# Kernel tuning notes

Hardware: AMD Instinct MI355X
Metric: run time of the kernel (lower is better)

## Reference

```python
import jax, jax.numpy as jnp
import numpy as np

D = 1024

def setup_inputs() -> dict:
    key = jax.random.key(0)
    k1, k2, k3, k4, k5 = jax.random.split(key, 5)
    B, S = 128, 512
    seq_output = jax.random.normal(k1, (B, S, D), dtype=jnp.float32)
    mask = jax.random.randint(k2, (B, S), 0, 2) == 1  # True = masked position
    # ensure last position is never fully-masked pathological: fine either way
    scale1 = 1.0 / np.sqrt(D)
    W1 = jax.random.normal(k3, (D, D), dtype=jnp.float32) * scale1
    b1 = jnp.zeros((D,), dtype=jnp.float32)
    w2 = jax.random.normal(k4, (D,), dtype=jnp.float32) * scale1
    return {"seq_output": seq_output, "mask": mask, "W1": W1, "b1": b1, "w2": w2}

def reference(seq_output, mask, W1, b1, w2):
    # u_last: last timestep embedding
    u_last = seq_output[:, -1, :]                           # [B, D]
    # additive attention MLP: Linear -> tanh -> Linear(D->1, no bias)
    h = jnp.tanh(jnp.einsum('bsd,de->bse', seq_output, W1) + b1)  # [B, S, D]
    scores = jnp.einsum('bsd,d->bs', h, w2)                 # [B, S]
    scores = jnp.where(mask, -1e9, scores)
    attn = jax.nn.softmax(scores, axis=-1)                  # [B, S]
    u_att = jnp.einsum('bs,bsd->bd', attn, seq_output)      # [B, D]
    return (u_last, u_att)
```

## Files before the change

### kernel.cpp

```cpp
#include <hip/hip_runtime.h>
#include <hip/hip_bf16.h>
#include <cstdint>
#include <cstddef>

#define BATCH 128
#define SEQ   512
#define DIM   1024
#define MROWS (BATCH * SEQ)
#define NT    32

typedef short short8 __attribute__((ext_vector_type(8)));
typedef __bf16 bf16x8 __attribute__((ext_vector_type(8)));
typedef float f32x4 __attribute__((ext_vector_type(4)));

template <typename VA> struct other_frag { using type = bf16x8; };
template <> struct other_frag<bf16x8> { using type = short8; };

template <typename VA>
__device__ __forceinline__ auto try_mfma(VA a, VA b, f32x4 c, int)
    -> decltype(__builtin_amdgcn_mfma_f32_16x16x32_bf16(a, b, c, 0, 0, 0)) {
  return __builtin_amdgcn_mfma_f32_16x16x32_bf16(a, b, c, 0, 0, 0);
}
template <typename VA>
__device__ __forceinline__ f32x4 try_mfma(VA a, VA b, f32x4 c, long) {
  using O = typename other_frag<VA>::type;
  O a2 = __builtin_bit_cast(O, a);
  O b2 = __builtin_bit_cast(O, b);
  return __builtin_amdgcn_mfma_f32_16x16x32_bf16(a2, b2, c, 0, 0, 0);
}
__device__ __forceinline__ f32x4 mfma_bf16(short8 a, short8 b, f32x4 c) {
  return try_mfma(a, b, c, 0);
}

__device__ __forceinline__ unsigned short f32_to_bf16(float f) {
  union { float f; uint32_t u; } v; v.f = f;
  uint32_t u = v.u;
  u += 0x7FFFu + ((u >> 16) & 1u);
  return (unsigned short)(u >> 16);
}

__device__ __forceinline__ float bf16_to_f32(unsigned short u) {
  union { uint32_t u; float f; } v; v.u = ((uint32_t)u) << 16; return v.f;
}

__device__ __forceinline__ void gload_lds16(const void* g, void* l) {
  __builtin_amdgcn_global_load_lds(
      (__attribute__((address_space(1))) void*)g,
      (__attribute__((address_space(3))) void*)l,
      16, 0, 0);
}

__device__ __forceinline__ float fast_tanh(float x) {
  x = fminf(fmaxf(x, -15.0f), 15.0f);
  float e = __expf(2.0f * x);
  return (e - 1.0f) / (e + 1.0f);
}

__global__ __launch_bounds__(256) void cast_x_kernel(const float* __restrict__ X,
                                                     unsigned short* __restrict__ Xb) {
  const int total8 = MROWS * DIM / 8;
  int idx = blockIdx.x * 256 + threadIdx.x;
  const int stride = 2048 * 256;
  for (int i = idx; i < total8; i += stride) {
    const f32x4* p = (const f32x4*)X + (size_t)i * 2;
    f32x4 a = p[0];
    f32x4 b = p[1];
    short8 o;
    o[0] = (short)f32_to_bf16(a[0]); o[1] = (short)f32_to_bf16(a[1]);
    o[2] = (short)f32_to_bf16(a[2]); o[3] = (short)f32_to_bf16(a[3]);
    o[4] = (short)f32_to_bf16(b[0]); o[5] = (short)f32_to_bf16(b[1]);
    o[6] = (short)f32_to_bf16(b[2]); o[7] = (short)f32_to_bf16(b[3]);
    *((short8*)Xb + i) = o;
  }
}

__global__ __launch_bounds__(256) void w1t_kernel(const float* __restrict__ W1,
                                                  unsigned short* __restrict__ W1t) {
  __shared__ float tile[64][65];
  int bx = blockIdx.x & 15;
  int by = blockIdx.x >> 4;
  int t = threadIdx.x;
  int c = t & 63, r0 = t >> 6;
#pragma unroll
  for (int i = 0; i < 16; i++) {
    int r = i * 4 + r0;
    tile[r][c] = W1[(size_t)(by * 64 + r) * DIM + bx * 64 + c];
  }
  __syncthreads();
#pragma unroll
  for (int i = 0; i < 16; i++) {
    int r = i * 4 + r0;
    W1t[(size_t)(bx * 64 + r) * DIM + by * 64 + c] = f32_to_bf16(tile[c][r]);
  }
}

__global__ __launch_bounds__(256) void ulast_kernel(const float* __restrict__ X,
                                                    float* __restrict__ u_last) {
  int i = blockIdx.x * 256 + threadIdx.x;
  int b = i >> 8;
  int d4 = i & 255;
  ((f32x4*)u_last)[i] = ((const f32x4*)X)[((size_t)b * SEQ + (SEQ - 1)) * 256 + d4];
}

__global__ __launch_bounds__(512, 2) void gemm_score_kernel(
    const unsigned short* __restrict__ Xb,
    const unsigned short* __restrict__ W1t,
    const float* __restrict__ b1,
    const float* __restrict__ w2,
    float* __restrict__ scores) {
  __shared__ __align__(16) char lds[131072];

  const int tid = threadIdx.x;
  const int lane = tid & 63;
  const int w = tid >> 6;
  const int wr = w >> 2, wc = w & 3;

  const int bx = blockIdx.x;
  const int swz = (bx & 7) * 128 + (bx >> 3);
  const int m0 = (swz >> 2) * 256;
  const int n0 = (swz & 3) * 256;

  const unsigned short *a0Src, *a1Src, *b0Src, *b1Src;
  {
    int sc0 = w * 64 + lane;
    int sr0 = sc0 >> 3, j0 = (sc0 & 7) ^ (sr0 & 7);
    int row0 = sr0 * 2 + (j0 >> 2), c40 = j0 & 3;
    a0Src = Xb  + (size_t)(m0 + row0) * DIM + c40 * 8;
    b0Src = W1t + (size_t)(n0 + row0) * DIM + c40 * 8;
    int sc1 = (8 + w) * 64 + lane;
    int sr1 = sc1 >> 3, j1 = (sc1 & 7) ^ (sr1 & 7);
    int row1 = sr1 * 2 + (j1 >> 2), c41 = j1 & 3;
    a1Src = Xb  + (size_t)(m0 + row1) * DIM + c41 * 8;
    b1Src = W1t + (size_t)(n0 + row1) * DIM + c41 * 8;
  }
  const int dst0 = w * 1024;
  const int dst1 = (8 + w) * 1024;

  int aOff[8];
#pragma unroll
  for (int mi = 0; mi < 8; mi++) {
    int row = wr * 128 + mi * 16 + (lane & 15);
    int srow = row >> 1;
    int ic = ((row & 1) * 4 + (lane >> 4)) ^ (srow & 7);
    aOff[mi] = srow * 128 + ic * 16;
  }
  int bOff[4];
#pragma unroll
  for (int ni = 0; ni < 4; ni++) {
    int row = wc * 64 + ni * 16 + (lane & 15);
    int srow = row >> 1;
    int ic = ((row & 1) * 4 + (lane >> 4)) ^ (srow & 7);
    bOff[ni] = 65536 + srow * 128 + ic * 16;
  }

  f32x4 acc[8][4];
#pragma unroll
  for (int mi = 0; mi < 8; mi++)
#pragma unroll
    for (int ni = 0; ni < 4; ni++)
      acc[mi][ni] = (f32x4){0.f, 0.f, 0.f, 0.f};

#define STAGE(S) do {                                                   \
    const int bufS_ = ((S) & 3) * 16384;                                \
    const int ktS_ = (S) * 32;                                          \
    gload_lds16(a0Src + ktS_, lds + bufS_ + dst0);                      \
    gload_lds16(a1Src + ktS_, lds + bufS_ + dst1);                      \
    gload_lds16(b0Src + ktS_, lds + 65536 + bufS_ + dst0);              \
    gload_lds16(b1Src + ktS_, lds + 65536 + bufS_ + dst1);              \
  } while (0)

#define KITER(S, VMSTR) do {                                            \
    asm volatile("s_waitcnt vmcnt(" VMSTR ")" ::: "memory");            \
    __builtin_amdgcn_s_barrier();                                       \
    __builtin_amdgcn_sched_barrier(0);                                  \
    if ((S) + 3 < NT) STAGE((S) + 3);                                   \
    const int buf_ = ((S) & 3) * 16384;                                 \
    short8 af[8], bfv[4];                                               \
    _Pragma("unroll")                                                   \
    for (int mi = 0; mi < 8; mi++)                                      \
      af[mi] = *(const short8*)(lds + buf_ + aOff[mi]);                 \
    _Pragma("unroll")                                                   \
    for (int ni = 0; ni < 4; ni++)                                      \
      bfv[ni] = *(const short8*)(lds + buf_ + bOff[ni]);                \
    __builtin_amdgcn_s_setprio(1);                                      \
    _Pragma("unroll")                                                   \
    for (int mi = 0; mi < 8; mi++)                                      \
      _Pragma("unroll")                                                 \
      for (int ni = 0; ni < 4; ni++)                                    \
        acc[mi][ni] = mfma_bf16(af[mi], bfv[ni], acc[mi][ni]);          \
    __builtin_amdgcn_s_setprio(0);                                      \
  } while (0)

  STAGE(0); STAGE(1); STAGE(2);

  for (int s = 0; s < NT - 2; ++s) KITER(s, "8");
  KITER(NT - 2, "4");
  KITER(NT - 1, "0");

#undef STAGE
#undef KITER

  const int cg = lane >> 4;
  const int cl = lane & 15;
#pragma unroll
  for (int mi = 0; mi < 8; mi++) {
    float p0 = 0.f, p1 = 0.f, p2 = 0.f, p3 = 0.f;
#pragma unroll
    for (int ni = 0; ni < 4; ni++) {
      int col = n0 + wc * 64 + ni * 16 + cl;
      float w2v = w2[col];
      float b1v = b1[col];
      p0 += fast_tanh(acc[mi][ni][0] + b1v) * w2v;
      p1 += fast_tanh(acc[mi][ni][1] + b1v) * w2v;
      p2 += fast_tanh(acc[mi][ni][2] + b1v) * w2v;
      p3 += fast_tanh(acc[mi][ni][3] + b1v) * w2v;
    }
#pragma unroll
    for (int off = 1; off < 16; off <<= 1) {
      p0 += __shfl_xor(p0, off);
      p1 += __shfl_xor(p1, off);
      p2 += __shfl_xor(p2, off);
      p3 += __shfl_xor(p3, off);
    }
    if (cl == 0) {
      int row = m0 + wr * 128 + mi * 16 + cg * 4;
      atomicAdd(&scores[row + 0], p0);
      atomicAdd(&scores[row + 1], p1);
      atomicAdd(&scores[row + 2], p2);
      atomicAdd(&scores[row + 3], p3);
    }
  }
}

__global__ __launch_bounds__(256) void attn_uatt_kernel(
    const unsigned short* __restrict__ Xb,
    const float* __restrict__ scores,
    const int* __restrict__ mask,
    float* __restrict__ u_att) {
  const int b = blockIdx.x;
  const int half = blockIdx.y;
  const int tid = threadIdx.x;
  const int lane = tid & 63;
  const int wave = tid >> 6;

  __shared__ float attn[SEQ];
  __shared__ float rbuf[4];
  __shared__ float part[3][64 * 9];

  float s0 = scores[(size_t)b * SEQ + tid];
  float s1 = scores[(size_t)b * SEQ + 256 + tid];
  if (mask[(size_t)b * SEQ + tid]) s0 = -1000000000.0f;
  if (mask[(size_t)b * SEQ + 256 + tid]) s1 = -1000000000.0f;

  float mx = fmaxf(s0, s1);
#pragma unroll
  for (int off = 1; off < 64; off <<= 1) mx = fmaxf(mx, __shfl_xor(mx, off));
  if (lane == 0) rbuf[wave] = mx;
  __syncthreads();
  mx = fmaxf(fmaxf(rbuf[0], rbuf[1]), fmaxf(rbuf[2], rbuf[3]));

  float p0 = expf(s0 - mx), p1 = expf(s1 - mx);
  float sm = p0 + p1;
#pragma unroll
  for (int off = 1; off < 64; off <<= 1) sm += __shfl_xor(sm, off);
  __syncthreads();
  if (lane == 0) rbuf[wave] = sm;
  __syncthreads();
  sm = rbuf[0] + rbuf[1] + rbuf[2] + rbuf[3];
  float inv = 1.0f / sm;
  attn[tid] = p0 * inv;
  attn[tid + 256] = p1 * inv;
  __syncthreads();

  const int col = tid & 63;
  const int sh = tid >> 6;
  const short8* Xp = (const short8*)Xb + (size_t)b * SEQ * (DIM / 8) + half * 64 + col;
  float a[8] = {0.f, 0.f, 0.f, 0.f, 0.f, 0.f, 0.f, 0.f};
  for (int s = sh * 128; s < sh * 128 + 128; s++) {
    short8 v = Xp[(size_t)s * (DIM / 8)];
    float wgt = attn[s];
#pragma unroll
    for (int j = 0; j < 8; j++)
      a[j] += wgt * bf16_to_f32((unsigned short)v[j]);
  }
  if (sh) {
#pragma unroll
    for (int j = 0; j < 8; j++) part[sh - 1][col * 9 + j] = a[j];
  }
  __syncthreads();
  if (sh == 0) {
#pragma unroll
    for (int j = 0; j < 8; j++)
      a[j] += part[0][col * 9 + j] + part[1][col * 9 + j] + part[2][col * 9 + j];
    f32x4 lo = {a[0], a[1], a[2], a[3]};
    f32x4 hi = {a[4], a[5], a[6], a[7]};
    f32x4* dst = (f32x4*)(u_att + (size_t)b * DIM + half * 512 + col * 8);
    dst[0] = lo;
    dst[1] = hi;
  }
}

extern "C" void kernel_launch(void* const* d_in, const int* in_sizes, int n_in,
                              void* d_out, int out_size, void* d_ws, size_t ws_size,
                              hipStream_t stream) {
  const float* X    = (const float*)d_in[0];
  const int*   mask = (const int*)d_in[1];
  const float* W1   = (const float*)d_in[2];
  const float* b1   = (const float*)d_in[3];
  const float* w2   = (const float*)d_in[4];

  float* out    = (float*)d_out;
  float* u_last = out;
  float* u_att  = out + BATCH * DIM;

  char* ws = (char*)d_ws;
  unsigned short* Xb  = (unsigned short*)ws;
  unsigned short* W1t = (unsigned short*)(ws + (size_t)MROWS * DIM * 2);
  float* scores = (float*)(ws + (size_t)MROWS * DIM * 2 + (size_t)DIM * DIM * 2);

  hipMemsetAsync(scores, 0, MROWS * sizeof(float), stream);
  hipLaunchKernelGGL(cast_x_kernel, dim3(2048), dim3(256), 0, stream, X, Xb);
  hipLaunchKernelGGL(w1t_kernel, dim3(256), dim3(256), 0, stream, W1, W1t);
  hipLaunchKernelGGL(ulast_kernel, dim3(128), dim3(256), 0, stream, X, u_last);
  hipLaunchKernelGGL(gemm_score_kernel, dim3(1024), dim3(512), 0, stream,
                     Xb, W1t, b1, w2, scores);
  hipLaunchKernelGGL(attn_uatt_kernel, dim3(128, 2), dim3(256), 0, stream,
                     Xb, scores, mask, u_att);
}
```

Measured before the change: 266.6 us.

## Use 64-wide K tiles with phased quarter-tile loads and fold u_last into cast

The GEMM main loop changes from 32-wide K stages in a 4-deep ring to 64-wide K tiles, double buffered. Each tile is split into four phases, and each phase issues part of the next tile's global-to-LDS loads interleaved with MFMA work, using a new XOR swizzle layout. B fragments are loaded once per tile and reused across the phases. Separately, the u_last copy is folded into the cast kernel, which removes one launch. The cost is an extra barrier per phase and a more intricate dependency schedule that is easy to get wrong.

```diff
diff --git a/kernel.cpp b/kernel.cpp
--- a/kernel.cpp
+++ b/kernel.cpp
@@ -7,7 +7,6 @@
 #define SEQ   512
 #define DIM   1024
 #define MROWS (BATCH * SEQ)
-#define NT    32
 
 typedef short short8 __attribute__((ext_vector_type(8)));
 typedef __bf16 bf16x8 __attribute__((ext_vector_type(8)));
@@ -57,7 +56,8 @@
 }
 
 __global__ __launch_bounds__(256) void cast_x_kernel(const float* __restrict__ X,
-                                                     unsigned short* __restrict__ Xb) {
+                                                     unsigned short* __restrict__ Xb,
+                                                     float* __restrict__ u_last) {
   const int total8 = MROWS * DIM / 8;
   int idx = blockIdx.x * 256 + threadIdx.x;
   const int stride = 2048 * 256;
@@ -71,6 +71,13 @@
     o[4] = (short)f32_to_bf16(b[0]); o[5] = (short)f32_to_bf16(b[1]);
     o[6] = (short)f32_to_bf16(b[2]); o[7] = (short)f32_to_bf16(b[3]);
     *((short8*)Xb + i) = o;
+    int row = i >> 7;
+    if ((row & (SEQ - 1)) == SEQ - 1) {
+      int g = i & 127;
+      f32x4* dst = (f32x4*)(u_last + (size_t)(row >> 9) * DIM + g * 8);
+      dst[0] = a;
+      dst[1] = b;
+    }
   }
 }
 
@@ -94,14 +101,6 @@
   }
 }
 
-__global__ __launch_bounds__(256) void ulast_kernel(const float* __restrict__ X,
-                                                    float* __restrict__ u_last) {
-  int i = blockIdx.x * 256 + threadIdx.x;
-  int b = i >> 8;
-  int d4 = i & 255;
-  ((f32x4*)u_last)[i] = ((const f32x4*)X)[((size_t)b * SEQ + (SEQ - 1)) * 256 + d4];
-}
-
 __global__ __launch_bounds__(512, 2) void gemm_score_kernel(
     const unsigned short* __restrict__ Xb,
     const unsigned short* __restrict__ W1t,
@@ -120,37 +119,51 @@
   const int m0 = (swz >> 2) * 256;
   const int n0 = (swz & 3) * 256;
 
-  const unsigned short *a0Src, *a1Src, *b0Src, *b1Src;
-  {
-    int sc0 = w * 64 + lane;
-    int sr0 = sc0 >> 3, j0 = (sc0 & 7) ^ (sr0 & 7);
-    int row0 = sr0 * 2 + (j0 >> 2), c40 = j0 & 3;
-    a0Src = Xb  + (size_t)(m0 + row0) * DIM + c40 * 8;
-    b0Src = W1t + (size_t)(n0 + row0) * DIM + c40 * 8;
-    int sc1 = (8 + w) * 64 + lane;
-    int sr1 = sc1 >> 3, j1 = (sc1 & 7) ^ (sr1 & 7);
-    int row1 = sr1 * 2 + (j1 >> 2), c41 = j1 & 3;
-    a1Src = Xb  + (size_t)(m0 + row1) * DIM + c41 * 8;
-    b1Src = W1t + (size_t)(n0 + row1) * DIM + c41 * 8;
-  }
-  const int dst0 = w * 1024;
-  const int dst1 = (8 + w) * 1024;
-
-  int aOff[8];
+#define FROW(r) (((r) & 7) ^ ((((r) >> 3) & 1) << 2))
+
+  const unsigned short *pAQ01[2], *pAQ23[2], *pBH0[2], *pBH1[2];
+#pragma unroll
+  for (int i = 0; i < 2; i++) {
+    int sc = i * 512 + tid;
+    int rr = sc >> 3, js = sc & 7;
+    int rA01 = rr + (rr & 64);
+    int rA23 = 64 + rr + (rr & 64);
+    int rB0 = rr;
+    int rB1 = 128 + rr;
+    pAQ01[i] = Xb  + (size_t)(m0 + rA01) * DIM + (js ^ FROW(rA01)) * 8;
+    pAQ23[i] = Xb  + (size_t)(m0 + rA23) * DIM + (js ^ FROW(rA23)) * 8;
+    pBH0[i]  = W1t + (size_t)(n0 + rB0) * DIM + (js ^ FROW(rB0)) * 8;
+    pBH1[i]  = W1t + (size_t)(n0 + rB1) * DIM + (js ^ FROW(rB1)) * 8;
+  }
+  int dA01[2], dA23[2], dB0[2], dB1[2];
+#pragma unroll
+  for (int i = 0; i < 2; i++) {
+    int rr0 = i * 64 + w * 8;
+    dA01[i] = (rr0 + (rr0 & 64)) * 128;
+    dA23[i] = (64 + rr0 + (rr0 & 64)) * 128;
+    dB0[i] = rr0 * 128;
+    dB1[i] = (128 + rr0) * 128;
+  }
+
+  int aOff[8][2];
 #pragma unroll
   for (int mi = 0; mi < 8; mi++) {
     int row = wr * 128 + mi * 16 + (lane & 15);
-    int srow = row >> 1;
-    int ic = ((row & 1) * 4 + (lane >> 4)) ^ (srow & 7);
-    aOff[mi] = srow * 128 + ic * 16;
-  }
-  int bOff[4];
+#pragma unroll
+    for (int kk = 0; kk < 2; kk++) {
+      int js = (kk * 4 + (lane >> 4)) ^ FROW(row);
+      aOff[mi][kk] = row * 128 + js * 16;
+    }
+  }
+  int bOff[4][2];
 #pragma unroll
   for (int ni = 0; ni < 4; ni++) {
     int row = wc * 64 + ni * 16 + (lane & 15);
-    int srow = row >> 1;
-    int ic = ((row & 1) * 4 + (lane >> 4)) ^ (srow & 7);
-    bOff[ni] = 65536 + srow * 128 + ic * 16;
+#pragma unroll
+    for (int kk = 0; kk < 2; kk++) {
+      int js = (kk * 4 + (lane >> 4)) ^ FROW(row);
+      bOff[ni][kk] = row * 128 + js * 16;
+    }
   }
 
   f32x4 acc[8][4];
@@ -160,45 +173,90 @@
     for (int ni = 0; ni < 4; ni++)
       acc[mi][ni] = (f32x4){0.f, 0.f, 0.f, 0.f};
 
-#define STAGE(S) do {                                                   \
-    const int bufS_ = ((S) & 3) * 16384;                                \
-    const int ktS_ = (S) * 32;                                          \
-    gload_lds16(a0Src + ktS_, lds + bufS_ + dst0);                      \
-    gload_lds16(a1Src + ktS_, lds + bufS_ + dst1);                      \
-    gload_lds16(b0Src + ktS_, lds + 65536 + bufS_ + dst0);              \
-    gload_lds16(b1Src + ktS_, lds + 65536 + bufS_ + dst1);              \
-  } while (0)
-
-#define KITER(S, VMSTR) do {                                            \
-    asm volatile("s_waitcnt vmcnt(" VMSTR ")" ::: "memory");            \
+  short8 bfv[4][2];
+
+#define ST_AQ01(T, BUF) do {                                            \
+    gload_lds16(pAQ01[0] + (T) * 64, lds + (BUF) * 32768 + dA01[0]);    \
+    gload_lds16(pAQ01[1] + (T) * 64, lds + (BUF) * 32768 + dA01[1]);    \
+  } while (0)
+#define ST_AQ23(T, BUF) do {                                            \
+    gload_lds16(pAQ23[0] + (T) * 64, lds + (BUF) * 32768 + dA23[0]);    \
+    gload_lds16(pAQ23[1] + (T) * 64, lds + (BUF) * 32768 + dA23[1]);    \
+  } while (0)
+#define ST_BH0(T, BUF) do {                                             \
+    gload_lds16(pBH0[0] + (T) * 64, lds + 65536 + (BUF) * 32768 + dB0[0]); \
+    gload_lds16(pBH0[1] + (T) * 64, lds + 65536 + (BUF) * 32768 + dB0[1]); \
+  } while (0)
+#define ST_BH1(T, BUF) do {                                             \
+    gload_lds16(pBH1[0] + (T) * 64, lds + 65536 + (BUF) * 32768 + dB1[0]); \
+    gload_lds16(pBH1[1] + (T) * 64, lds + 65536 + (BUF) * 32768 + dB1[1]); \
+  } while (0)
+
+#define PHASE(T, BUF, Q, STAGE, WAIT) do {                              \
+    const char* bufA_ = lds + (BUF) * 32768;                            \
+    short8 af0_ = *(const short8*)(bufA_ + aOff[2 * (Q)][0]);           \
+    short8 af1_ = *(const short8*)(bufA_ + aOff[2 * (Q)][1]);           \
+    short8 af2_ = *(const short8*)(bufA_ + aOff[2 * (Q) + 1][0]);       \
+    short8 af3_ = *(const short8*)(bufA_ + aOff[2 * (Q) + 1][1]);       \
+    if ((Q) == 0) {                                                     \
+      const char* bufB_ = lds + 65536 + (BUF) * 32768;                  \
+      _Pragma("unroll")                                                 \
+      for (int ni = 0; ni < 4; ni++) {                                  \
+        bfv[ni][0] = *(const short8*)(bufB_ + bOff[ni][0]);             \
+        bfv[ni][1] = *(const short8*)(bufB_ + bOff[ni][1]);             \
+      }                                                                 \
+    }                                                                   \
+    STAGE;                                                              \
     __builtin_amdgcn_s_barrier();                                       \
-    __builtin_amdgcn_sched_barrier(0);                                  \
-    if ((S) + 3 < NT) STAGE((S) + 3);                                   \
-    const int buf_ = ((S) & 3) * 16384;                                 \
-    short8 af[8], bfv[4];                                               \
-    _Pragma("unroll")                                                   \
-    for (int mi = 0; mi < 8; mi++)                                      \
-      af[mi] = *(const short8*)(lds + buf_ + aOff[mi]);                 \
-    _Pragma("unroll")                                                   \
-    for (int ni = 0; ni < 4; ni++)                                      \
-      bfv[ni] = *(const short8*)(lds + buf_ + bOff[ni]);                \
     __builtin_amdgcn_s_setprio(1);                                      \
     _Pragma("unroll")                                                   \
-    for (int mi = 0; mi < 8; mi++)                                      \
-      _Pragma("unroll")                                                 \
-      for (int ni = 0; ni < 4; ni++)                                    \
-        acc[mi][ni] = mfma_bf16(af[mi], bfv[ni], acc[mi][ni]);          \
+    for (int ni = 0; ni < 4; ni++) {                                    \
+      acc[2 * (Q)][ni] = mfma_bf16(af0_, bfv[ni][0], acc[2 * (Q)][ni]); \
+      acc[2 * (Q)][ni] = mfma_bf16(af1_, bfv[ni][1], acc[2 * (Q)][ni]); \
+      acc[2 * (Q) + 1][ni] = mfma_bf16(af2_, bfv[ni][0], acc[2 * (Q) + 1][ni]); \
+      acc[2 * (Q) + 1][ni] = mfma_bf16(af3_, bfv[ni][1], acc[2 * (Q) + 1][ni]); \
+    }                                                                   \
     __builtin_amdgcn_s_setprio(0);                                      \
-  } while (0)
-
-  STAGE(0); STAGE(1); STAGE(2);
-
-  for (int s = 0; s < NT - 2; ++s) KITER(s, "8");
-  KITER(NT - 2, "4");
-  KITER(NT - 1, "0");
-
-#undef STAGE
-#undef KITER
+    WAIT;                                                               \
+    __builtin_amdgcn_s_barrier();                                       \
+  } while (0)
+
+#define NOP_ do {} while (0)
+#define WAIT6 asm volatile("s_waitcnt vmcnt(6)" ::: "memory")
+#define WAIT0 asm volatile("s_waitcnt vmcnt(0)" ::: "memory")
+
+#define TILE_FULL(T, BUF, OBUF) do {                                    \
+    PHASE(T, BUF, 0, ST_AQ23((T) + 1, OBUF), NOP_);                     \
+    PHASE(T, BUF, 1, ST_BH0((T) + 2, BUF), NOP_);                       \
+    PHASE(T, BUF, 2, ST_BH1((T) + 2, BUF), NOP_);                       \
+    PHASE(T, BUF, 3, ST_AQ01((T) + 2, BUF), WAIT6);                     \
+  } while (0)
+
+  ST_AQ01(0, 0); ST_AQ23(0, 0); ST_BH0(0, 0); ST_BH1(0, 0);
+  ST_BH0(1, 1);  ST_BH1(1, 1);  ST_AQ01(1, 1);
+  WAIT6;
+  __builtin_amdgcn_s_barrier();
+
+  for (int t = 0; t < 7; ++t) {
+    const int T0 = 2 * t;
+    TILE_FULL(T0, 0, 1);
+    TILE_FULL(T0 + 1, 1, 0);
+  }
+  PHASE(14, 0, 0, ST_AQ23(15, 1), NOP_);
+  PHASE(14, 0, 1, NOP_, NOP_);
+  PHASE(14, 0, 2, NOP_, NOP_);
+  PHASE(14, 0, 3, NOP_, WAIT0);
+  PHASE(15, 1, 0, NOP_, NOP_);
+  PHASE(15, 1, 1, NOP_, NOP_);
+  PHASE(15, 1, 2, NOP_, NOP_);
+  PHASE(15, 1, 3, NOP_, NOP_);
+
+#undef TILE_FULL
+#undef PHASE
+#undef ST_AQ01
+#undef ST_AQ23
+#undef ST_BH0
+#undef ST_BH1
 
   const int cg = lane >> 4;
   const int cl = lane & 15;
@@ -319,9 +377,8 @@
   float* scores = (float*)(ws + (size_t)MROWS * DIM * 2 + (size_t)DIM * DIM * 2);
 
   hipMemsetAsync(scores, 0, MROWS * sizeof(float), stream);
-  hipLaunchKernelGGL(cast_x_kernel, dim3(2048), dim3(256), 0, stream, X, Xb);
+  hipLaunchKernelGGL(cast_x_kernel, dim3(2048), dim3(256), 0, stream, X, Xb, u_last);
   hipLaunchKernelGGL(w1t_kernel, dim3(256), dim3(256), 0, stream, W1, W1t);
-  hipLaunchKernelGGL(ulast_kernel, dim3(128), dim3(256), 0, stream, X, u_last);
   hipLaunchKernelGGL(gemm_score_kernel, dim3(1024), dim3(512), 0, stream,
                      Xb, W1t, b1, w2, scores);
   hipLaunchKernelGGL(attn_uatt_kernel, dim3(128, 2), dim3(256), 0, stream,
```

Result: slower. 276.2 us (+3.6%).
